# Optimization experiments

Hardware: AMD Instinct MI355X
Metric: run time of the kernel (lower is better)

Reference implementation:

```python
import jax, jax.numpy as jnp
import numpy as np

TEMP = 0.1
EPS = 1e-12  # torch F.normalize eps


def _normalize(v):
    return v / jnp.maximum(jnp.linalg.norm(v, axis=1, keepdims=True), EPS)


def _scale_loss(a1, a2, b1, c1):
    # diag of exp(a1 @ a2.T / temp): computed directly from paired rows
    # (same math as eye-mask + row-sum in the original).
    diag = jnp.exp(jnp.sum(a1 * a2, axis=1) / TEMP)            # [B]
    denom = (jnp.exp(a1 @ b1.T / TEMP).sum(1, keepdims=True)
             + jnp.exp(a1 @ c1.T / TEMP).sum(1, keepdims=True))  # [B,1]
    # NOTE: [B] / [B,1] broadcasts to [B,B], exactly as in the torch code.
    return jnp.mean(-jnp.log(diag / denom))


def setup_inputs() -> dict:
    key = jax.random.key(0)
    kx, ky, kz = jax.random.split(key, 3)
    shape = (8192, 128)
    return {
        "x": jax.random.normal(kx, shape, dtype=jnp.float32),
        "y": jax.random.normal(ky, shape, dtype=jnp.float32),
        "z": jax.random.normal(kz, shape, dtype=jnp.float32),
    }


def reference(x, y, z):
    x = _normalize(x)
    y = _normalize(y)
    z = _normalize(z)
    B = x.shape[0] // 2
    x1, x2 = x[:B], x[B:]
    y1, y2 = y[:B], y[B:]
    z1, z2 = z[:B], z[B:]

    loss_scale = (_scale_loss(x1, x2, y1, z1)
                  + _scale_loss(y1, y2, x1, z1)
                  + _scale_loss(z1, z2, x1, y1))

    xyz1 = jnp.concatenate([x1, y1, z1], axis=1)  # [B, 3D]
    xyz2 = jnp.concatenate([x2, y2, z2], axis=1)
    m = jnp.exp(xyz1 @ xyz2.T / TEMP)             # [B, B]
    # [B] / [B,1] -> [B,B] broadcast, matching the torch code.
    loss_view = jnp.mean(-jnp.log(jnp.diagonal(m) / m.sum(1, keepdims=True)))

    return loss_view + loss_scale
```

## Files before the change

### kernel.cpp

```cpp
#include <hip/hip_runtime.h>
#include <hip/hip_bf16.h>

#define BHALF 4096
#define DDIM 128
#define KCAT 384
#define TEMP_INV 10.0f
#define EXP2K 14.426950408889634f

typedef __attribute__((ext_vector_type(8))) short short8;
typedef __attribute__((ext_vector_type(4))) float f32x4;

__device__ __forceinline__ void gload16(const ushort* g, ushort* l) {
  __builtin_amdgcn_global_load_lds(
      (const __attribute__((address_space(1))) unsigned int*)g,
      (__attribute__((address_space(3))) unsigned int*)l, 16, 0, 0);
}

__global__ __launch_bounds__(256) void norm_diag_kernel(
    const float* __restrict__ x, const float* __restrict__ y,
    const float* __restrict__ z, ushort* __restrict__ nrm1,
    ushort* __restrict__ nrm2, float* __restrict__ dxyz) {
  int wave = threadIdx.x >> 6;
  int lane = threadIdx.x & 63;
  int gi = blockIdx.x * 4 + wave;
  int mat = gi >> 12;
  int i = gi & 4095;
  const float* src = (mat == 0 ? x : (mat == 1 ? y : z));
  float2 a = *(const float2*)(src + (size_t)i * DDIM + lane * 2);
  float2 b = *(const float2*)(src + (size_t)(i + BHALF) * DDIM + lane * 2);
  float s1 = a.x * a.x + a.y * a.y;
  float s2 = b.x * b.x + b.y * b.y;
  float d = a.x * b.x + a.y * b.y;
#pragma unroll
  for (int m = 1; m < 64; m <<= 1) {
    s1 += __shfl_xor(s1, m, 64);
    s2 += __shfl_xor(s2, m, 64);
    d += __shfl_xor(d, m, 64);
  }
  float r1 = 1.0f / fmaxf(sqrtf(s1), 1e-12f);
  float r2 = 1.0f / fmaxf(sqrtf(s2), 1e-12f);
  ushort* d1 = nrm1 + (size_t)i * KCAT + mat * DDIM + lane * 2;
  ushort* d2 = nrm2 + (size_t)i * KCAT + mat * DDIM + lane * 2;
  __hip_bfloat162 o1, o2;
  o1.x = __float2bfloat16(a.x * r1);
  o1.y = __float2bfloat16(a.y * r1);
  o2.x = __float2bfloat16(b.x * r2);
  o2.y = __float2bfloat16(b.y * r2);
  *(__hip_bfloat162*)d1 = o1;
  *(__hip_bfloat162*)d2 = o2;
  if (lane == 0) dxyz[mat * BHALF + i] = d * r1 * r2;
}


__device__ __forceinline__ void flush_cheap(f32x4 (&acc)[4][4],
                                            float* __restrict__ dst, int base,
                                            int lane) {
#pragma unroll
  for (int m = 0; m < 4; ++m) {
    float s = 0.0f;
#pragma unroll
    for (int n = 0; n < 4; ++n)
#pragma unroll
      for (int r = 0; r < 4; ++r) s += exp2f(acc[m][n][r] * EXP2K);
    s += __shfl_xor(s, 16, 64);
    s += __shfl_xor(s, 32, 64);
    if (lane < 16) atomicAdd(&dst[base + m * 16 + lane], s);
  }
}

__device__ __forceinline__ void flush_full(f32x4 (&acc)[4][4],
                                           float* __restrict__ rs,
                                           float* __restrict__ cs, int rbase,
                                           int cbase, int lane) {
#pragma unroll
  for (int m = 0; m < 4; ++m)
#pragma unroll
    for (int n = 0; n < 4; ++n)
#pragma unroll
      for (int r = 0; r < 4; ++r)
        acc[m][n][r] = exp2f(acc[m][n][r] * EXP2K);

#pragma unroll
  for (int m = 0; m < 4; ++m) {
    float rsum[4];
#pragma unroll
    for (int r = 0; r < 4; ++r)
      rsum[r] = acc[m][0][r] + acc[m][1][r] + acc[m][2][r] + acc[m][3][r];
#pragma unroll
    for (int r = 0; r < 4; ++r) {
      rsum[r] += __shfl_xor(rsum[r], 1, 64);
      rsum[r] += __shfl_xor(rsum[r], 2, 64);
      rsum[r] += __shfl_xor(rsum[r], 4, 64);
      rsum[r] += __shfl_xor(rsum[r], 8, 64);
    }
    if ((lane & 15) == 0) {
      int rb = rbase + m * 16 + (lane >> 4) * 4;
#pragma unroll
      for (int r = 0; r < 4; ++r) atomicAdd(&rs[rb + r], rsum[r]);
    }
  }

#pragma unroll
  for (int n = 0; n < 4; ++n) {
    float csum = 0.0f;
#pragma unroll
    for (int m = 0; m < 4; ++m)
#pragma unroll
      for (int r = 0; r < 4; ++r) csum += acc[m][n][r];
    csum += __shfl_xor(csum, 16, 64);
    csum += __shfl_xor(csum, 32, 64);
    if (lane < 16) atomicAdd(&cs[cbase + n * 16 + lane], csum);
  }
}

__global__ __launch_bounds__(256) void gram_slab_kernel(
    const ushort* __restrict__ nrm1, const ushort* __restrict__ nrm2,
    float* __restrict__ sums) {
  __shared__ ushort As[4][128][32];
  __shared__ ushort Bs[4][128][32];

  int tid = threadIdx.x;
  int lane = tid & 63;
  int wave = tid >> 6;
  int wr = wave >> 1;
  int wc = wave & 1;
  int g = (blockIdx.z == 0) ? 3 : (int)blockIdx.z - 1;
  int rowbase = blockIdx.x * 128;
  int colbase = blockIdx.y * 128;

  const ushort* Ab;
  const ushort* Bb;
  int nslab;
  float* rs;
  float* cs;
  if (g == 3) {
    Ab = nrm1;       Bb = nrm2;       nslab = 3;
    rs = sums + 6 * 4096; cs = nullptr;
  } else if (g == 0) {
    Ab = nrm1;       Bb = nrm1 + 128; nslab = 1;
    rs = sums;            cs = sums + 4096;
  } else if (g == 1) {
    Ab = nrm1;       Bb = nrm1 + 256; nslab = 1;
    rs = sums + 2 * 4096; cs = sums + 3 * 4096;
  } else {
    Ab = nrm1 + 128; Bb = nrm1 + 256; nslab = 1;
    rs = sums + 4 * 4096; cs = sums + 5 * 4096;
  }

  int srow = lane >> 2;
  int schunk = ((lane & 3) ^ ((lane >> 3) & 3)) << 3;
  const ushort* gA =
      Ab + (size_t)(rowbase + wave * 32 + srow) * KCAT + schunk;
  const ushort* gB =
      Bb + (size_t)(colbase + wave * 32 + srow) * KCAT + schunk;

  int rsel = lane & 15;
  int slot8 = (((lane >> 4) ^ ((rsel >> 1) & 3)) << 3);

  f32x4 acc[4][4] = {};

  for (int slab = 0; slab < nslab; ++slab) {
    if (slab) {
      __builtin_amdgcn_s_barrier();
      __builtin_amdgcn_sched_barrier(0);
    }
    int k0 = slab * 128;
#pragma unroll
    for (int s = 0; s < 4; ++s) {
#pragma unroll
      for (int rg = 0; rg < 2; ++rg) {
        gload16(gA + k0 + s * 32 + (size_t)rg * 16 * KCAT,
                &As[s][wave * 32 + rg * 16][0]);
        gload16(gB + k0 + s * 32 + (size_t)rg * 16 * KCAT,
                &Bs[s][wave * 32 + rg * 16][0]);
      }
    }
    asm volatile("s_waitcnt vmcnt(0)" ::: "memory");
    __builtin_amdgcn_s_barrier();
    __builtin_amdgcn_sched_barrier(0);

    if (g == 3) {
#pragma unroll
      for (int kk = 0; kk < 4; ++kk) {
        short8 af[4], bf[4];
#pragma unroll
        for (int m = 0; m < 4; ++m)
          af[m] = *(const short8*)&As[kk][wr * 64 + m * 16 + rsel][slot8];
#pragma unroll
        for (int n = 0; n < 4; ++n)
          bf[n] = *(const short8*)&Bs[kk][wc * 64 + n * 16 + rsel][slot8];
#pragma unroll
        for (int m = 0; m < 4; ++m)
#pragma unroll
          for (int n = 0; n < 4; ++n)
            acc[m][n] = __builtin_amdgcn_mfma_f32_16x16x32_bf16(
                bf[n], af[m], acc[m][n], 0, 0, 0);
      }
    } else {
#pragma unroll
      for (int kk = 0; kk < 4; ++kk) {
        short8 af[4], bf[4];
#pragma unroll
        for (int m = 0; m < 4; ++m)
          af[m] = *(const short8*)&As[kk][wr * 64 + m * 16 + rsel][slot8];
#pragma unroll
        for (int n = 0; n < 4; ++n)
          bf[n] = *(const short8*)&Bs[kk][wc * 64 + n * 16 + rsel][slot8];
#pragma unroll
        for (int m = 0; m < 4; ++m)
#pragma unroll
          for (int n = 0; n < 4; ++n)
            acc[m][n] = __builtin_amdgcn_mfma_f32_16x16x32_bf16(
                af[m], bf[n], acc[m][n], 0, 0, 0);
      }
    }
  }

  if (g == 3)
    flush_cheap(acc, rs, rowbase + wr * 64, lane);
  else
    flush_full(acc, rs, cs, rowbase + wr * 64, colbase + wc * 64, lane);
}

__global__ __launch_bounds__(1024) void loss_kernel(
    const float* __restrict__ sums, const float* __restrict__ dxyz,
    float* __restrict__ out) {
  const float* rs0 = sums;
  const float* cs0 = sums + 4096;
  const float* rs1 = sums + 2 * 4096;
  const float* cs1 = sums + 3 * 4096;
  const float* rs2 = sums + 4 * 4096;
  const float* cs2 = sums + 5 * 4096;
  const float* rs3 = sums + 6 * 4096;
  int tid = threadIdx.x;
  float acc = 0.0f;
  for (int i = tid; i < BHALF; i += 1024) {
    float dxv = dxyz[i];
    float dyv = dxyz[4096 + i];
    float dzv = dxyz[2 * 4096 + i];
    float lx = logf(rs0[i] + rs1[i]) - TEMP_INV * dxv;
    float ly = logf(cs0[i] + rs2[i]) - TEMP_INV * dyv;
    float lz = logf(cs1[i] + cs2[i]) - TEMP_INV * dzv;
    float lv = logf(rs3[i]) - TEMP_INV * (dxv + dyv + dzv);
    acc += lx + ly + lz + lv;
  }
  __shared__ float red[16];
#pragma unroll
  for (int m = 1; m < 64; m <<= 1) acc += __shfl_xor(acc, m, 64);
  if ((tid & 63) == 0) red[tid >> 6] = acc;
  __syncthreads();
  if (tid == 0) {
    float t = 0.0f;
#pragma unroll
    for (int i = 0; i < 16; ++i) t += red[i];
    out[0] = t * (1.0f / 4096.0f);
  }
}

extern "C" void kernel_launch(void* const* d_in, const int* in_sizes, int n_in,
                              void* d_out, int out_size, void* d_ws,
                              size_t ws_size, hipStream_t stream) {
  const float* x = (const float*)d_in[0];
  const float* y = (const float*)d_in[1];
  const float* z = (const float*)d_in[2];
  char* ws = (char*)d_ws;
  ushort* nrm1 = (ushort*)ws;
  ushort* nrm2 = nrm1 + (size_t)BHALF * KCAT;
  float* sums = (float*)(ws + 2 * (size_t)BHALF * KCAT * sizeof(ushort));
  float* dxyz = sums + 7 * 4096;

  hipMemsetAsync(sums, 0, 7 * 4096 * sizeof(float), stream);
  norm_diag_kernel<<<3 * BHALF / 4, 256, 0, stream>>>(x, y, z, nrm1, nrm2,
                                                      dxyz);
  gram_slab_kernel<<<dim3(32, 32, 4), 256, 0, stream>>>(nrm1, nrm2, sums);
  loss_kernel<<<1, 1024, 0, stream>>>(sums, dxyz, (float*)d_out);
}
```

Measured before the change: 76.95 us.

## Load MFMA operands directly from global memory instead of staging through LDS

The gram kernel no longer stages tiles through shared memory with global_load_lds and barriers. Each wave now reads its bf16 A and B fragments straight from global memory into registers. This removes the LDS traffic, the barriers and the waitcnt stalls, and frees LDS so more blocks can be resident. The cost is redundant global/L2 reads, since tiles are no longer shared across waves, and loads that are less coalesced (16-byte chunks spread over 16 rows).

```diff
diff --git a/kernel.cpp b/kernel.cpp
--- a/kernel.cpp
+++ b/kernel.cpp
@@ -9,12 +9,6 @@
 
 typedef __attribute__((ext_vector_type(8))) short short8;
 typedef __attribute__((ext_vector_type(4))) float f32x4;
-
-__device__ __forceinline__ void gload16(const ushort* g, ushort* l) {
-  __builtin_amdgcn_global_load_lds(
-      (const __attribute__((address_space(1))) unsigned int*)g,
-      (__attribute__((address_space(3))) unsigned int*)l, 16, 0, 0);
-}
 
 __global__ __launch_bounds__(256) void norm_diag_kernel(
     const float* __restrict__ x, const float* __restrict__ y,
@@ -113,12 +107,9 @@
   }
 }
 
-__global__ __launch_bounds__(256) void gram_slab_kernel(
+__global__ __launch_bounds__(256) void gram_direct_kernel(
     const ushort* __restrict__ nrm1, const ushort* __restrict__ nrm2,
     float* __restrict__ sums) {
-  __shared__ ushort As[4][128][32];
-  __shared__ ushort Bs[4][128][32];
-
   int tid = threadIdx.x;
   int lane = tid & 63;
   int wave = tid >> 6;
@@ -130,89 +121,65 @@
 
   const ushort* Ab;
   const ushort* Bb;
-  int nslab;
+  int nsteps;
   float* rs;
   float* cs;
   if (g == 3) {
-    Ab = nrm1;       Bb = nrm2;       nslab = 3;
+    Ab = nrm1;       Bb = nrm2;       nsteps = 12;
     rs = sums + 6 * 4096; cs = nullptr;
   } else if (g == 0) {
-    Ab = nrm1;       Bb = nrm1 + 128; nslab = 1;
+    Ab = nrm1;       Bb = nrm1 + 128; nsteps = 4;
     rs = sums;            cs = sums + 4096;
   } else if (g == 1) {
-    Ab = nrm1;       Bb = nrm1 + 256; nslab = 1;
+    Ab = nrm1;       Bb = nrm1 + 256; nsteps = 4;
     rs = sums + 2 * 4096; cs = sums + 3 * 4096;
   } else {
-    Ab = nrm1 + 128; Bb = nrm1 + 256; nslab = 1;
+    Ab = nrm1 + 128; Bb = nrm1 + 256; nsteps = 4;
     rs = sums + 4 * 4096; cs = sums + 5 * 4096;
   }
 
-  int srow = lane >> 2;
-  int schunk = ((lane & 3) ^ ((lane >> 3) & 3)) << 3;
-  const ushort* gA =
-      Ab + (size_t)(rowbase + wave * 32 + srow) * KCAT + schunk;
-  const ushort* gB =
-      Bb + (size_t)(colbase + wave * 32 + srow) * KCAT + schunk;
-
   int rsel = lane & 15;
-  int slot8 = (((lane >> 4) ^ ((rsel >> 1) & 3)) << 3);
+  int fc8 = (lane >> 4) * 8;
+  const ushort* aP[4];
+  const ushort* bP[4];
+#pragma unroll
+  for (int m = 0; m < 4; ++m)
+    aP[m] = Ab + (size_t)(rowbase + wr * 64 + m * 16 + rsel) * KCAT + fc8;
+#pragma unroll
+  for (int n = 0; n < 4; ++n)
+    bP[n] = Bb + (size_t)(colbase + wc * 64 + n * 16 + rsel) * KCAT + fc8;
 
   f32x4 acc[4][4] = {};
 
-  for (int slab = 0; slab < nslab; ++slab) {
-    if (slab) {
-      __builtin_amdgcn_s_barrier();
-      __builtin_amdgcn_sched_barrier(0);
-    }
-    int k0 = slab * 128;
-#pragma unroll
-    for (int s = 0; s < 4; ++s) {
-#pragma unroll
-      for (int rg = 0; rg < 2; ++rg) {
-        gload16(gA + k0 + s * 32 + (size_t)rg * 16 * KCAT,
-                &As[s][wave * 32 + rg * 16][0]);
-        gload16(gB + k0 + s * 32 + (size_t)rg * 16 * KCAT,
-                &Bs[s][wave * 32 + rg * 16][0]);
-      }
-    }
-    asm volatile("s_waitcnt vmcnt(0)" ::: "memory");
-    __builtin_amdgcn_s_barrier();
-    __builtin_amdgcn_sched_barrier(0);
-
-    if (g == 3) {
-#pragma unroll
-      for (int kk = 0; kk < 4; ++kk) {
-        short8 af[4], bf[4];
-#pragma unroll
-        for (int m = 0; m < 4; ++m)
-          af[m] = *(const short8*)&As[kk][wr * 64 + m * 16 + rsel][slot8];
+  if (g == 3) {
+#pragma unroll 2
+    for (int t = 0; t < 12; ++t) {
+      short8 af[4], bf[4];
+#pragma unroll
+      for (int m = 0; m < 4; ++m) af[m] = *(const short8*)(aP[m] + t * 32);
+#pragma unroll
+      for (int n = 0; n < 4; ++n) bf[n] = *(const short8*)(bP[n] + t * 32);
+#pragma unroll
+      for (int m = 0; m < 4; ++m)
 #pragma unroll
         for (int n = 0; n < 4; ++n)
-          bf[n] = *(const short8*)&Bs[kk][wc * 64 + n * 16 + rsel][slot8];
-#pragma unroll
-        for (int m = 0; m < 4; ++m)
-#pragma unroll
-          for (int n = 0; n < 4; ++n)
-            acc[m][n] = __builtin_amdgcn_mfma_f32_16x16x32_bf16(
-                bf[n], af[m], acc[m][n], 0, 0, 0);
-      }
-    } else {
-#pragma unroll
-      for (int kk = 0; kk < 4; ++kk) {
-        short8 af[4], bf[4];
-#pragma unroll
-        for (int m = 0; m < 4; ++m)
-          af[m] = *(const short8*)&As[kk][wr * 64 + m * 16 + rsel][slot8];
+          acc[m][n] = __builtin_amdgcn_mfma_f32_16x16x32_bf16(
+              bf[n], af[m], acc[m][n], 0, 0, 0);
+    }
+  } else {
+#pragma unroll
+    for (int t = 0; t < 4; ++t) {
+      short8 af[4], bf[4];
+#pragma unroll
+      for (int m = 0; m < 4; ++m) af[m] = *(const short8*)(aP[m] + t * 32);
+#pragma unroll
+      for (int n = 0; n < 4; ++n) bf[n] = *(const short8*)(bP[n] + t * 32);
+#pragma unroll
+      for (int m = 0; m < 4; ++m)
 #pragma unroll
         for (int n = 0; n < 4; ++n)
-          bf[n] = *(const short8*)&Bs[kk][wc * 64 + n * 16 + rsel][slot8];
-#pragma unroll
-        for (int m = 0; m < 4; ++m)
-#pragma unroll
-          for (int n = 0; n < 4; ++n)
-            acc[m][n] = __builtin_amdgcn_mfma_f32_16x16x32_bf16(
-                af[m], bf[n], acc[m][n], 0, 0, 0);
-      }
+          acc[m][n] = __builtin_amdgcn_mfma_f32_16x16x32_bf16(
+              af[m], bf[n], acc[m][n], 0, 0, 0);
     }
   }
 
@@ -272,6 +239,6 @@
   hipMemsetAsync(sums, 0, 7 * 4096 * sizeof(float), stream);
   norm_diag_kernel<<<3 * BHALF / 4, 256, 0, stream>>>(x, y, z, nrm1, nrm2,
                                                       dxyz);
-  gram_slab_kernel<<<dim3(32, 32, 4), 256, 0, stream>>>(nrm1, nrm2, sums);
+  gram_direct_kernel<<<dim3(32, 32, 4), 256, 0, stream>>>(nrm1, nrm2, sums);
   loss_kernel<<<1, 1024, 0, stream>>>(sums, dxyz, (float*)d_out);
 }
```

Result: slower. 158.9 us (+106.5%).

## Switch normalized operands and Gram MFMAs from bf16 to fp8 e4m3

Applied to the files above, without the earlier changes.

Normalized rows are now stored as fp8 e4m3 instead of bf16, halving workspace traffic and LDS footprint. The Gram kernel uses fp8 MFMA (16x16x32 fp8) with a new single-stage 128x128-byte LDS layout and a new XOR swizzle. This roughly doubles MFMA throughput and halves load bytes. The cost is much lower precision on dot products that are then scaled by 10 and exponentiated, which risks accuracy failures.

```diff
diff --git a/kernel.cpp b/kernel.cpp
--- a/kernel.cpp
+++ b/kernel.cpp
@@ -1,5 +1,6 @@
 #include <hip/hip_runtime.h>
 #include <hip/hip_bf16.h>
+#include <hip/hip_fp8.h>
 
 #define BHALF 4096
 #define DDIM 128
@@ -7,10 +8,10 @@
 #define TEMP_INV 10.0f
 #define EXP2K 14.426950408889634f
 
-typedef __attribute__((ext_vector_type(8))) short short8;
+typedef unsigned char u8;
 typedef __attribute__((ext_vector_type(4))) float f32x4;
 
-__device__ __forceinline__ void gload16(const ushort* g, ushort* l) {
+__device__ __forceinline__ void gload16(const u8* g, u8* l) {
   __builtin_amdgcn_global_load_lds(
       (const __attribute__((address_space(1))) unsigned int*)g,
       (__attribute__((address_space(3))) unsigned int*)l, 16, 0, 0);
@@ -18,8 +19,8 @@
 
 __global__ __launch_bounds__(256) void norm_diag_kernel(
     const float* __restrict__ x, const float* __restrict__ y,
-    const float* __restrict__ z, ushort* __restrict__ nrm1,
-    ushort* __restrict__ nrm2, float* __restrict__ dxyz) {
+    const float* __restrict__ z, u8* __restrict__ nrm1, u8* __restrict__ nrm2,
+    float* __restrict__ dxyz) {
   int wave = threadIdx.x >> 6;
   int lane = threadIdx.x & 63;
   int gi = blockIdx.x * 4 + wave;
@@ -39,15 +40,12 @@
   }
   float r1 = 1.0f / fmaxf(sqrtf(s1), 1e-12f);
   float r2 = 1.0f / fmaxf(sqrtf(s2), 1e-12f);
-  ushort* d1 = nrm1 + (size_t)i * KCAT + mat * DDIM + lane * 2;
-  ushort* d2 = nrm2 + (size_t)i * KCAT + mat * DDIM + lane * 2;
-  __hip_bfloat162 o1, o2;
-  o1.x = __float2bfloat16(a.x * r1);
-  o1.y = __float2bfloat16(a.y * r1);
-  o2.x = __float2bfloat16(b.x * r2);
-  o2.y = __float2bfloat16(b.y * r2);
-  *(__hip_bfloat162*)d1 = o1;
-  *(__hip_bfloat162*)d2 = o2;
+  __hip_fp8_e4m3 qa0(a.x * r1), qa1(a.y * r1);
+  __hip_fp8_e4m3 qb0(b.x * r2), qb1(b.y * r2);
+  ushort pa = (ushort)qa0.__x | ((ushort)qa1.__x << 8);
+  ushort pb = (ushort)qb0.__x | ((ushort)qb1.__x << 8);
+  *(ushort*)(nrm1 + (size_t)i * KCAT + mat * DDIM + lane * 2) = pa;
+  *(ushort*)(nrm2 + (size_t)i * KCAT + mat * DDIM + lane * 2) = pb;
   if (lane == 0) dxyz[mat * BHALF + i] = d * r1 * r2;
 }
 
@@ -114,10 +112,10 @@
 }
 
 __global__ __launch_bounds__(256) void gram_slab_kernel(
-    const ushort* __restrict__ nrm1, const ushort* __restrict__ nrm2,
+    const u8* __restrict__ nrm1, const u8* __restrict__ nrm2,
     float* __restrict__ sums) {
-  __shared__ ushort As[4][128][32];
-  __shared__ ushort Bs[4][128][32];
+  __shared__ u8 As[128][128];
+  __shared__ u8 Bs[128][128];
 
   int tid = threadIdx.x;
   int lane = tid & 63;
@@ -128,8 +126,8 @@
   int rowbase = blockIdx.x * 128;
   int colbase = blockIdx.y * 128;
 
-  const ushort* Ab;
-  const ushort* Bb;
+  const u8* Ab;
+  const u8* Bb;
   int nslab;
   float* rs;
   float* cs;
@@ -147,15 +145,16 @@
     rs = sums + 4 * 4096; cs = sums + 5 * 4096;
   }
 
-  int srow = lane >> 2;
-  int schunk = ((lane & 3) ^ ((lane >> 3) & 3)) << 3;
-  const ushort* gA =
-      Ab + (size_t)(rowbase + wave * 32 + srow) * KCAT + schunk;
-  const ushort* gB =
-      Bb + (size_t)(colbase + wave * 32 + srow) * KCAT + schunk;
+  int srow = lane >> 3;
+  int sslot = ((lane & 7) ^ srow) << 4;
+  const u8* gA = Ab + (size_t)(rowbase + wave * 32 + srow) * KCAT + sslot;
+  const u8* gB = Bb + (size_t)(colbase + wave * 32 + srow) * KCAT + sslot;
 
   int rsel = lane & 15;
-  int slot8 = (((lane >> 4) ^ ((rsel >> 1) & 3)) << 3);
+  int r7 = rsel & 7;
+  int fc = lane >> 4;
+  int sub8 = (fc & 1) << 3;
+  int s16 = fc >> 1;
 
   f32x4 acc[4][4] = {};
 
@@ -166,52 +165,38 @@
     }
     int k0 = slab * 128;
 #pragma unroll
-    for (int s = 0; s < 4; ++s) {
-#pragma unroll
-      for (int rg = 0; rg < 2; ++rg) {
-        gload16(gA + k0 + s * 32 + (size_t)rg * 16 * KCAT,
-                &As[s][wave * 32 + rg * 16][0]);
-        gload16(gB + k0 + s * 32 + (size_t)rg * 16 * KCAT,
-                &Bs[s][wave * 32 + rg * 16][0]);
-      }
+    for (int ld = 0; ld < 4; ++ld) {
+      gload16(gA + k0 + (size_t)ld * 8 * KCAT, &As[wave * 32 + ld * 8][0]);
+      gload16(gB + k0 + (size_t)ld * 8 * KCAT, &Bs[wave * 32 + ld * 8][0]);
     }
     asm volatile("s_waitcnt vmcnt(0)" ::: "memory");
     __builtin_amdgcn_s_barrier();
     __builtin_amdgcn_sched_barrier(0);
 
-    if (g == 3) {
-#pragma unroll
-      for (int kk = 0; kk < 4; ++kk) {
-        short8 af[4], bf[4];
+#pragma unroll
+    for (int kk = 0; kk < 4; ++kk) {
+      long long a8[4], b8[4];
+      int off = (((kk * 2 + s16) ^ r7) << 4) + sub8;
+#pragma unroll
+      for (int m = 0; m < 4; ++m)
+        a8[m] = *(const long long*)&As[wr * 64 + m * 16 + rsel][off];
+#pragma unroll
+      for (int n = 0; n < 4; ++n)
+        b8[n] = *(const long long*)&Bs[wc * 64 + n * 16 + rsel][off];
+      if (g == 3) {
 #pragma unroll
         for (int m = 0; m < 4; ++m)
-          af[m] = *(const short8*)&As[kk][wr * 64 + m * 16 + rsel][slot8];
-#pragma unroll
-        for (int n = 0; n < 4; ++n)
-          bf[n] = *(const short8*)&Bs[kk][wc * 64 + n * 16 + rsel][slot8];
+#pragma unroll
+          for (int n = 0; n < 4; ++n)
+            acc[m][n] = __builtin_amdgcn_mfma_f32_16x16x32_fp8_fp8(
+                b8[n], a8[m], acc[m][n], 0, 0, 0);
+      } else {
 #pragma unroll
         for (int m = 0; m < 4; ++m)
 #pragma unroll
           for (int n = 0; n < 4; ++n)
-            acc[m][n] = __builtin_amdgcn_mfma_f32_16x16x32_bf16(
-                bf[n], af[m], acc[m][n], 0, 0, 0);
-      }
-    } else {
-#pragma unroll
-      for (int kk = 0; kk < 4; ++kk) {
-        short8 af[4], bf[4];
-#pragma unroll
-        for (int m = 0; m < 4; ++m)
-          af[m] = *(const short8*)&As[kk][wr * 64 + m * 16 + rsel][slot8];
-#pragma unroll
-        for (int n = 0; n < 4; ++n)
-          bf[n] = *(const short8*)&Bs[kk][wc * 64 + n * 16 + rsel][slot8];
-#pragma unroll
-        for (int m = 0; m < 4; ++m)
-#pragma unroll
-          for (int n = 0; n < 4; ++n)
-            acc[m][n] = __builtin_amdgcn_mfma_f32_16x16x32_bf16(
-                af[m], bf[n], acc[m][n], 0, 0, 0);
+            acc[m][n] = __builtin_amdgcn_mfma_f32_16x16x32_fp8_fp8(
+                a8[m], b8[n], acc[m][n], 0, 0, 0);
       }
     }
   }
@@ -264,9 +249,9 @@
   const float* y = (const float*)d_in[1];
   const float* z = (const float*)d_in[2];
   char* ws = (char*)d_ws;
-  ushort* nrm1 = (ushort*)ws;
-  ushort* nrm2 = nrm1 + (size_t)BHALF * KCAT;
-  float* sums = (float*)(ws + 2 * (size_t)BHALF * KCAT * sizeof(ushort));
+  u8* nrm1 = (u8*)ws;
+  u8* nrm2 = nrm1 + (size_t)BHALF * KCAT;
+  float* sums = (float*)(ws + 2 * (size_t)BHALF * KCAT);
   float* dxyz = sums + 7 * 4096;
 
   hipMemsetAsync(sums, 0, 7 * 4096 * sizeof(float), stream);
```

Measured after the change: 99.03 us. 28.7% more time.

## Replace global atomics with per-tile partial sums reduced in loss kernel

Applied to the files above, without the earlier changes.

The gram kernel now writes its row and column exp-sums into per-tile partial buffers instead of issuing float atomicAdds into shared sum arrays. The loss kernel is spread over 16 blocks, reduces the 64 partials per row, and combines its block results with one atomic on the output. This removes atomic contention and the memset of the sums buffer. In exchange it writes and reads about 7 MB of partial data and needs a much larger workspace.

```diff
diff --git a/kernel.cpp b/kernel.cpp
--- a/kernel.cpp
+++ b/kernel.cpp
@@ -6,6 +6,7 @@
 #define KCAT 384
 #define TEMP_INV 10.0f
 #define EXP2K 14.426950408889634f
+#define PSTRIDE (64 * 4096)
 
 typedef __attribute__((ext_vector_type(8))) short short8;
 typedef __attribute__((ext_vector_type(4))) float f32x4;
@@ -64,7 +65,7 @@
       for (int r = 0; r < 4; ++r) s += exp2f(acc[m][n][r] * EXP2K);
     s += __shfl_xor(s, 16, 64);
     s += __shfl_xor(s, 32, 64);
-    if (lane < 16) atomicAdd(&dst[base + m * 16 + lane], s);
+    if (lane < 16) dst[base + m * 16 + lane] = s;
   }
 }
 
@@ -96,7 +97,7 @@
     if ((lane & 15) == 0) {
       int rb = rbase + m * 16 + (lane >> 4) * 4;
 #pragma unroll
-      for (int r = 0; r < 4; ++r) atomicAdd(&rs[rb + r], rsum[r]);
+      for (int r = 0; r < 4; ++r) rs[rb + r] = rsum[r];
     }
   }
 
@@ -109,13 +110,13 @@
       for (int r = 0; r < 4; ++r) csum += acc[m][n][r];
     csum += __shfl_xor(csum, 16, 64);
     csum += __shfl_xor(csum, 32, 64);
-    if (lane < 16) atomicAdd(&cs[cbase + n * 16 + lane], csum);
+    if (lane < 16) cs[cbase + n * 16 + lane] = csum;
   }
 }
 
 __global__ __launch_bounds__(256) void gram_slab_kernel(
     const ushort* __restrict__ nrm1, const ushort* __restrict__ nrm2,
-    float* __restrict__ sums) {
+    float* __restrict__ parts) {
   __shared__ ushort As[4][128][32];
   __shared__ ushort Bs[4][128][32];
 
@@ -125,26 +126,30 @@
   int wr = wave >> 1;
   int wc = wave & 1;
   int g = (blockIdx.z == 0) ? 3 : (int)blockIdx.z - 1;
-  int rowbase = blockIdx.x * 128;
-  int colbase = blockIdx.y * 128;
+  int bi = blockIdx.x;
+  int bj = blockIdx.y;
+  int rowbase = bi * 128;
+  int colbase = bj * 128;
 
   const ushort* Ab;
   const ushort* Bb;
   int nslab;
   float* rs;
   float* cs;
+  int rslot = (bj * 2 + wc) * 4096;
+  int cslot = (bi * 2 + wr) * 4096;
   if (g == 3) {
     Ab = nrm1;       Bb = nrm2;       nslab = 3;
-    rs = sums + 6 * 4096; cs = nullptr;
+    rs = parts + 6 * PSTRIDE + rslot; cs = nullptr;
   } else if (g == 0) {
     Ab = nrm1;       Bb = nrm1 + 128; nslab = 1;
-    rs = sums;            cs = sums + 4096;
+    rs = parts + 0 * PSTRIDE + rslot; cs = parts + 1 * PSTRIDE + cslot;
   } else if (g == 1) {
     Ab = nrm1;       Bb = nrm1 + 256; nslab = 1;
-    rs = sums + 2 * 4096; cs = sums + 3 * 4096;
+    rs = parts + 2 * PSTRIDE + rslot; cs = parts + 3 * PSTRIDE + cslot;
   } else {
     Ab = nrm1 + 128; Bb = nrm1 + 256; nslab = 1;
-    rs = sums + 4 * 4096; cs = sums + 5 * 4096;
+    rs = parts + 4 * PSTRIDE + rslot; cs = parts + 5 * PSTRIDE + cslot;
   }
 
   int srow = lane >> 2;
@@ -222,39 +227,30 @@
     flush_full(acc, rs, cs, rowbase + wr * 64, colbase + wc * 64, lane);
 }
 
-__global__ __launch_bounds__(1024) void loss_kernel(
-    const float* __restrict__ sums, const float* __restrict__ dxyz,
+__global__ __launch_bounds__(256) void loss_kernel(
+    const float* __restrict__ parts, const float* __restrict__ dxyz,
     float* __restrict__ out) {
-  const float* rs0 = sums;
-  const float* cs0 = sums + 4096;
-  const float* rs1 = sums + 2 * 4096;
-  const float* cs1 = sums + 3 * 4096;
-  const float* rs2 = sums + 4 * 4096;
-  const float* cs2 = sums + 5 * 4096;
-  const float* rs3 = sums + 6 * 4096;
-  int tid = threadIdx.x;
-  float acc = 0.0f;
-  for (int i = tid; i < BHALF; i += 1024) {
-    float dxv = dxyz[i];
-    float dyv = dxyz[4096 + i];
-    float dzv = dxyz[2 * 4096 + i];
-    float lx = logf(rs0[i] + rs1[i]) - TEMP_INV * dxv;
-    float ly = logf(cs0[i] + rs2[i]) - TEMP_INV * dyv;
-    float lz = logf(cs1[i] + cs2[i]) - TEMP_INV * dzv;
-    float lv = logf(rs3[i]) - TEMP_INV * (dxv + dyv + dzv);
-    acc += lx + ly + lz + lv;
-  }
-  __shared__ float red[16];
+  int i = blockIdx.x * 256 + threadIdx.x;
+  float s[7] = {0, 0, 0, 0, 0, 0, 0};
+  for (int p = 0; p < 64; ++p) {
+#pragma unroll
+    for (int a = 0; a < 7; ++a) s[a] += parts[a * PSTRIDE + p * 4096 + i];
+  }
+  float dxv = dxyz[i];
+  float dyv = dxyz[4096 + i];
+  float dzv = dxyz[2 * 4096 + i];
+  float lx = logf(s[0] + s[2]) - TEMP_INV * dxv;
+  float ly = logf(s[1] + s[4]) - TEMP_INV * dyv;
+  float lz = logf(s[3] + s[5]) - TEMP_INV * dzv;
+  float lv = logf(s[6]) - TEMP_INV * (dxv + dyv + dzv);
+  float acc = (lx + ly + lz + lv) * (1.0f / 4096.0f);
 #pragma unroll
   for (int m = 1; m < 64; m <<= 1) acc += __shfl_xor(acc, m, 64);
-  if ((tid & 63) == 0) red[tid >> 6] = acc;
+  __shared__ float red[4];
+  if ((threadIdx.x & 63) == 0) red[threadIdx.x >> 6] = acc;
   __syncthreads();
-  if (tid == 0) {
-    float t = 0.0f;
-#pragma unroll
-    for (int i = 0; i < 16; ++i) t += red[i];
-    out[0] = t * (1.0f / 4096.0f);
-  }
+  if (threadIdx.x == 0)
+    atomicAdd(out, red[0] + red[1] + red[2] + red[3]);
 }
 
 extern "C" void kernel_launch(void* const* d_in, const int* in_sizes, int n_in,
@@ -266,12 +262,12 @@
   char* ws = (char*)d_ws;
   ushort* nrm1 = (ushort*)ws;
   ushort* nrm2 = nrm1 + (size_t)BHALF * KCAT;
-  float* sums = (float*)(ws + 2 * (size_t)BHALF * KCAT * sizeof(ushort));
-  float* dxyz = sums + 7 * 4096;
-
-  hipMemsetAsync(sums, 0, 7 * 4096 * sizeof(float), stream);
+  float* parts = (float*)(ws + 2 * (size_t)BHALF * KCAT * sizeof(ushort));
+  float* dxyz = parts + 7 * PSTRIDE;
+
+  hipMemsetAsync(d_out, 0, sizeof(float), stream);
   norm_diag_kernel<<<3 * BHALF / 4, 256, 0, stream>>>(x, y, z, nrm1, nrm2,
                                                       dxyz);
-  gram_slab_kernel<<<dim3(32, 32, 4), 256, 0, stream>>>(nrm1, nrm2, sums);
-  loss_kernel<<<1, 1024, 0, stream>>>(sums, dxyz, (float*)d_out);
-}
+  gram_slab_kernel<<<dim3(32, 32, 4), 256, 0, stream>>>(nrm1, nrm2, parts);
+  loss_kernel<<<16, 256, 0, stream>>>(parts, dxyz, (float*)d_out);
+}
```

Result: no change. 78.17 us (+1.6%).
